# Kernel tuning notes

Hardware: AMD Instinct MI355X
Metric: run time of the kernel (lower is better)

Reference implementation:

```python
import jax, jax.numpy as jnp
import numpy as np

B, NX, NY, H = 4096, 64, 64, 256
ITERS = 20
REG = 0.1          # SinkhornScorer reg (stored as log, used as exp(log reg))
TEMP = 0.1         # SinkhornScorer temperature
ALPHA_BOTH = -100.0
LN_EPS = 1e-5


def setup_inputs() -> dict:
    key = jax.random.key(0)
    k1, k2, k3 = jax.random.split(key, 3)
    return {
        "x": jax.random.normal(k1, (B, NX, H), dtype=jnp.float32),
        "y": jax.random.normal(k2, (B, NY, H), dtype=jnp.float32),
        "ln_gamma": jnp.ones((H,), dtype=jnp.float32),
        "ln_beta": jnp.zeros((H,), dtype=jnp.float32),
        "w_db": jax.random.normal(k3, (H, 1), dtype=jnp.float32) * 0.05,
        "b_db": jnp.zeros((1,), dtype=jnp.float32),
    }


def _layer_norm(t, g, b):
    mu = jnp.mean(t, axis=-1, keepdims=True)
    var = jnp.mean((t - mu) ** 2, axis=-1, keepdims=True)  # biased, like torch LayerNorm
    return (t - mu) / jnp.sqrt(var + LN_EPS) * g + b


def _l2norm(t):
    n = jnp.sqrt(jnp.sum(t * t, axis=-1, keepdims=True))
    return t / jnp.maximum(n, 1e-12)


def reference(x, y, ln_gamma, ln_beta, w_db, b_db):
    b, m, h = x.shape
    n = y.shape[1]
    log_reg = jnp.log(jnp.float32(REG))
    log_temp = jnp.log(jnp.float32(TEMP))

    # CosineScorer(temperature=1), get_diag=False -> (b, n_x, n_y)
    scores = jnp.einsum("bxh,byh->bxy", _l2norm(x), _l2norm(y))

    # dustbin scores: tanh(Linear(LayerNorm(.))) -> (b, n, 1)
    alpha_x = jnp.tanh(_layer_norm(x, ln_gamma, ln_beta) @ w_db + b_db)  # (b, m, 1)
    alpha_y = jnp.tanh(_layer_norm(y, ln_gamma, ln_beta) @ w_db + b_db)  # (b, n, 1)

    # --- log_optimal_transport (SuperGlue-style with per-element dustbins) ---
    top = jnp.concatenate([scores, alpha_x], axis=2)                     # (b, m, n+1)
    bot = jnp.concatenate(
        [jnp.swapaxes(alpha_y, 1, 2), jnp.full((b, 1, 1), ALPHA_BOTH, scores.dtype)],
        axis=2,
    )                                                                    # (b, 1, n+1)
    couplings = jnp.concatenate([top, bot], axis=1) / jnp.exp(log_reg)   # (b, m+1, n+1)

    norm = -jnp.log(jnp.float32(m + n))
    log_mu = jnp.concatenate(
        [jnp.full((m,), norm), jnp.array([jnp.log(jnp.float32(n)) + norm])]
    )
    log_nu = jnp.concatenate(
        [jnp.full((n,), norm), jnp.array([jnp.log(jnp.float32(m)) + norm])]
    )
    log_mu = jnp.broadcast_to(log_mu, (b, m + 1))
    log_nu = jnp.broadcast_to(log_nu, (b, n + 1))

    def step(carry, _):
        u, v = carry
        u = log_mu - jax.nn.logsumexp(couplings + v[:, None, :], axis=2)
        v = log_nu - jax.nn.logsumexp(couplings + u[:, :, None], axis=1)
        return (u, v), None

    (u, v), _ = jax.lax.scan(
        step, (jnp.zeros_like(log_mu), jnp.zeros_like(log_nu)), None, length=ITERS
    )

    matching = couplings + u[:, :, None] + v[:, None, :] - norm  # log matching, (b, m+1, n+1)
    # per-pair alignment score: expected cosine similarity under the plan, / temperature
    score_out = jnp.sum(jnp.exp(matching[:, :-1, :-1]) * scores, axis=(1, 2)) / jnp.exp(log_temp)
    return matching, score_out
```

## Files before the change

kernel.cpp:

```cpp
#include <hip/hip_runtime.h>

#define NR 64
#define NH 256
#define NP1 65
#define TSTRIDE 68
#define NITER 20

__device__ __forceinline__ float dot4(float4 a, float4 b) {
  return a.x * b.x + a.y * b.y + a.z * b.z + a.w * b.w;
}

__global__ __launch_bounds__(256, 4)
void sinkhorn_kernel(const float* __restrict__ x, const float* __restrict__ y,
                     const float* __restrict__ gam, const float* __restrict__ bet,
                     const float* __restrict__ wdb, const float* __restrict__ bdb,
                     float* __restrict__ out_match, float* __restrict__ out_score)
{
  const int b    = blockIdx.x;
  const int t    = threadIdx.x;
  const int lane = t & 63;
  const int wvid = t >> 6;
  const int ti   = t >> 4;
  const int tj   = t & 15;
  const int i0   = ti * 4, j0 = tj * 4;

  __shared__ __align__(16) float s_buf[2 * NR * TSTRIDE];
  __shared__ __align__(16) float s_gw[NH];
  __shared__ __align__(16) float s_sx[NR], s_ax[NR], s_sy[NR], s_ay[NR];
  __shared__ float s_red[8];
  __shared__ float s_S12[2];

  float* xsT  = s_buf;
  float* ysT  = s_buf + NR * TSTRIDE;
  float* vp   = s_buf;
  float* vp64 = s_buf + 512;

  const float norm_c  = -4.852030263919617f;
  const float logmu64 = -0.6931471805599453f;

  {
    float gv = gam[t];
    float wv = wdb[t];
    float p1 = gv * wv;
    float p2 = bet[t] * wv;
    s_gw[t] = p1;
    #pragma unroll
    for (int o = 1; o < 64; o <<= 1) { p1 += __shfl_xor(p1, o); p2 += __shfl_xor(p2, o); }
    if (lane == 0) { s_red[wvid * 2] = p1; s_red[wvid * 2 + 1] = p2; }
  }
  __syncthreads();
  if (t == 0) {
    s_S12[0] = s_red[0] + s_red[2] + s_red[4] + s_red[6];
    s_S12[1] = s_red[1] + s_red[3] + s_red[5] + s_red[7] + bdb[0];
  }

  float acc[4][4] = {};
  float xsum[4] = {}, xsq[4] = {}, xdg[4] = {};
  float ysum[4] = {}, ysq[4] = {}, ydg[4] = {};

  const size_t gbase = (size_t)b * NR * NH;
  const int lh4 = tj * 4;

  for (int ch = 0; ch < 4; ++ch) {
    __syncthreads();
    const float4 gw4 = *(const float4*)(s_gw + ch * 64 + lh4);
    #pragma unroll
    for (int j = 0; j < 4; ++j) {
      const int row = ti + 16 * j;
      const int wcol = ((((row >> 2) ^ tj) & 15) << 2) + (row & 3);
      const float4 xv = *(const float4*)(x + gbase + (size_t)row * NH + ch * 64 + lh4);
      xsum[j] += xv.x + xv.y + xv.z + xv.w;
      xsq[j]  += dot4(xv, xv);
      xdg[j]  += dot4(xv, gw4);
      xsT[(lh4 + 0) * TSTRIDE + wcol] = xv.x;
      xsT[(lh4 + 1) * TSTRIDE + wcol] = xv.y;
      xsT[(lh4 + 2) * TSTRIDE + wcol] = xv.z;
      xsT[(lh4 + 3) * TSTRIDE + wcol] = xv.w;
      const float4 yv = *(const float4*)(y + gbase + (size_t)row * NH + ch * 64 + lh4);
      ysum[j] += yv.x + yv.y + yv.z + yv.w;
      ysq[j]  += dot4(yv, yv);
      ydg[j]  += dot4(yv, gw4);
      ysT[(lh4 + 0) * TSTRIDE + wcol] = yv.x;
      ysT[(lh4 + 1) * TSTRIDE + wcol] = yv.y;
      ysT[(lh4 + 2) * TSTRIDE + wcol] = yv.z;
      ysT[(lh4 + 3) * TSTRIDE + wcol] = yv.w;
    }
    __syncthreads();
    #pragma unroll 4
    for (int k = 0; k < 64; ++k) {
      const int kb = k >> 2;
      const float4 a4 = *(const float4*)(xsT + k * TSTRIDE + (((ti ^ kb) & 15) << 2));
      const float4 b4 = *(const float4*)(ysT + k * TSTRIDE + (((tj ^ kb) & 15) << 2));
      acc[0][0] += a4.x * b4.x; acc[0][1] += a4.x * b4.y; acc[0][2] += a4.x * b4.z; acc[0][3] += a4.x * b4.w;
      acc[1][0] += a4.y * b4.x; acc[1][1] += a4.y * b4.y; acc[1][2] += a4.y * b4.z; acc[1][3] += a4.y * b4.w;
      acc[2][0] += a4.z * b4.x; acc[2][1] += a4.z * b4.y; acc[2][2] += a4.z * b4.z; acc[2][3] += a4.z * b4.w;
      acc[3][0] += a4.w * b4.x; acc[3][1] += a4.w * b4.y; acc[3][2] += a4.w * b4.z; acc[3][3] += a4.w * b4.w;
    }
  }

  #pragma unroll
  for (int o = 1; o < 16; o <<= 1) {
    #pragma unroll
    for (int j = 0; j < 4; ++j) {
      xsum[j] += __shfl_xor(xsum[j], o);
      xsq[j]  += __shfl_xor(xsq[j], o);
      xdg[j]  += __shfl_xor(xdg[j], o);
      ysum[j] += __shfl_xor(ysum[j], o);
      ysq[j]  += __shfl_xor(ysq[j], o);
      ydg[j]  += __shfl_xor(ydg[j], o);
    }
  }
  {
    if (tj == 0) {
      const float S1 = s_S12[0], S2 = s_S12[1];
      #pragma unroll
      for (int j = 0; j < 4; ++j) {
        const int r = ti + 16 * j;
        float mu   = xsum[j] * (1.0f / NH);
        float var  = xsq[j] * (1.0f / NH) - mu * mu;
        float rstd = rsqrtf(var + 1e-5f);
        s_ax[r] = tanhf(rstd * (xdg[j] - mu * S1) + S2);
        s_sx[r] = 1.0f / fmaxf(sqrtf(xsq[j]), 1e-12f);
        mu   = ysum[j] * (1.0f / NH);
        var  = ysq[j] * (1.0f / NH) - mu * mu;
        rstd = rsqrtf(var + 1e-5f);
        s_ay[r] = tanhf(rstd * (ydg[j] - mu * S1) + S2);
        s_sy[r] = 1.0f / fmaxf(sqrtf(ysq[j]), 1e-12f);
      }
    }
  }
  __syncthreads();

  const float4 sx4 = *(const float4*)(s_sx + i0);
  const float4 sy4 = *(const float4*)(s_sy + j0);
  const float4 ax4 = *(const float4*)(s_ax + i0);
  const float4 ay4 = *(const float4*)(s_ay + j0);
  const float sxr[4] = {sx4.x, sx4.y, sx4.z, sx4.w};
  const float syc[4] = {sy4.x, sy4.y, sy4.z, sy4.w};
  float C[4][4], E[4][4];
  #pragma unroll
  for (int r = 0; r < 4; ++r) {
    #pragma unroll
    for (int c = 0; c < 4; ++c) {
      C[r][c] = acc[r][c] * sxr[r] * syc[c] * 10.0f;
      E[r][c] = __expf(C[r][c]);
    }
  }
  const float exi64[4] = {__expf(10.0f * ax4.x), __expf(10.0f * ax4.y),
                          __expf(10.0f * ax4.z), __expf(10.0f * ax4.w)};
  const float ey64[4]  = {__expf(10.0f * ay4.x), __expf(10.0f * ay4.y),
                          __expf(10.0f * ay4.z), __expf(10.0f * ay4.w)};

  float ev_c[4] = {1.0f, 1.0f, 1.0f, 1.0f};
  float ev64 = 1.0f;
  float eu_r[4];
  float eu64 = 1.0f;
  float su_s[4], p64_s, sv_s[4], rs_s;
  int bufo = 0;

  #pragma unroll 2
  for (int it = 0; it < NITER; ++it) {
    float s0 = E[0][0] * ev_c[0] + E[0][1] * ev_c[1] + E[0][2] * ev_c[2] + E[0][3] * ev_c[3];
    float s1 = E[1][0] * ev_c[0] + E[1][1] * ev_c[1] + E[1][2] * ev_c[2] + E[1][3] * ev_c[3];
    float s2 = E[2][0] * ev_c[0] + E[2][1] * ev_c[1] + E[2][2] * ev_c[2] + E[2][3] * ev_c[3];
    float s3 = E[3][0] * ev_c[0] + E[3][1] * ev_c[1] + E[3][2] * ev_c[2] + E[3][3] * ev_c[3];
    float p64 = ey64[0] * ev_c[0] + ey64[1] * ev_c[1] + ey64[2] * ev_c[2] + ey64[3] * ev_c[3];
    #pragma unroll
    for (int o = 1; o < 16; o <<= 1) {
      s0  += __shfl_xor(s0, o);
      s1  += __shfl_xor(s1, o);
      s2  += __shfl_xor(s2, o);
      s3  += __shfl_xor(s3, o);
      p64 += __shfl_xor(p64, o);
    }
    su_s[0] = s0 + exi64[0] * ev64;
    su_s[1] = s1 + exi64[1] * ev64;
    su_s[2] = s2 + exi64[2] * ev64;
    su_s[3] = s3 + exi64[3] * ev64;
    p64_s = p64;
    eu_r[0] = 0.0078125f * __builtin_amdgcn_rcpf(su_s[0]);
    eu_r[1] = 0.0078125f * __builtin_amdgcn_rcpf(su_s[1]);
    eu_r[2] = 0.0078125f * __builtin_amdgcn_rcpf(su_s[2]);
    eu_r[3] = 0.0078125f * __builtin_amdgcn_rcpf(su_s[3]);
    eu64    = 0.5f       * __builtin_amdgcn_rcpf(p64);

    float q0 = E[0][0] * eu_r[0] + E[1][0] * eu_r[1] + E[2][0] * eu_r[2] + E[3][0] * eu_r[3];
    float q1 = E[0][1] * eu_r[0] + E[1][1] * eu_r[1] + E[2][1] * eu_r[2] + E[3][1] * eu_r[3];
    float q2 = E[0][2] * eu_r[0] + E[1][2] * eu_r[1] + E[2][2] * eu_r[2] + E[3][2] * eu_r[3];
    float q3 = E[0][3] * eu_r[0] + E[1][3] * eu_r[1] + E[2][3] * eu_r[2] + E[3][3] * eu_r[3];
    float r64 = exi64[0] * eu_r[0] + exi64[1] * eu_r[1] + exi64[2] * eu_r[2] + exi64[3] * eu_r[3];
    #pragma unroll
    for (int o = 16; o < 64; o <<= 1) {
      q0  += __shfl_xor(q0, o);
      q1  += __shfl_xor(q1, o);
      q2  += __shfl_xor(q2, o);
      q3  += __shfl_xor(q3, o);
      r64 += __shfl_xor(r64, o);
    }
    if ((t & 48) == 0) {
      *(float4*)(vp + (bufo * 4 + wvid) * 64 + j0) = make_float4(q0, q1, q2, q3);
      if (tj == 0) vp64[bufo * 4 + wvid] = r64;
    }
    __syncthreads();
    float sv0 = 0.0f, sv1 = 0.0f, sv2 = 0.0f, sv3 = 0.0f;
    #pragma unroll
    for (int w = 0; w < 4; ++w) {
      const float4 qq = *(const float4*)(vp + (bufo * 4 + w) * 64 + j0);
      sv0 += qq.x; sv1 += qq.y; sv2 += qq.z; sv3 += qq.w;
    }
    const float4 rr4 = *(const float4*)(vp64 + bufo * 4);
    rs_s = rr4.x + rr4.y + rr4.z + rr4.w;
    sv_s[0] = sv0 + ey64[0] * eu64;
    sv_s[1] = sv1 + ey64[1] * eu64;
    sv_s[2] = sv2 + ey64[2] * eu64;
    sv_s[3] = sv3 + ey64[3] * eu64;
    ev_c[0] = 0.0078125f * __builtin_amdgcn_rcpf(sv_s[0]);
    ev_c[1] = 0.0078125f * __builtin_amdgcn_rcpf(sv_s[1]);
    ev_c[2] = 0.0078125f * __builtin_amdgcn_rcpf(sv_s[2]);
    ev_c[3] = 0.0078125f * __builtin_amdgcn_rcpf(sv_s[3]);
    ev64    = 0.5f       * __builtin_amdgcn_rcpf(rs_s);
    bufo ^= 1;
  }

  float u_r[4], v_c[4];
  #pragma unroll
  for (int r = 0; r < 4; ++r) u_r[r] = norm_c - __logf(su_s[r]);
  #pragma unroll
  for (int c = 0; c < 4; ++c) v_c[c] = norm_c - __logf(sv_s[c]);
  const float u64 = logmu64 - __logf(p64_s);
  const float v64 = logmu64 - __logf(rs_s);

  float sacc = 0.0f;
  const size_t mbase = (size_t)b * (size_t)(NP1 * NP1);
  #pragma unroll
  for (int r = 0; r < 4; ++r) {
    const float m0 = C[r][0] + u_r[r] + v_c[0] - norm_c;
    const float m1 = C[r][1] + u_r[r] + v_c[1] - norm_c;
    const float m2 = C[r][2] + u_r[r] + v_c[2] - norm_c;
    const float m3 = C[r][3] + u_r[r] + v_c[3] - norm_c;
    *(float4*)(out_match + mbase + (size_t)(i0 + r) * NP1 + j0) = make_float4(m0, m1, m2, m3);
    sacc += __expf(m0) * C[r][0] + __expf(m1) * C[r][1]
          + __expf(m2) * C[r][2] + __expf(m3) * C[r][3];
  }
  if (t < 16) {
    const float4 ayv = *(const float4*)(s_ay + j0);
    *(float4*)(out_match + mbase + (size_t)64 * NP1 + j0) = make_float4(
        10.0f * ayv.x + u64 + v_c[0] - norm_c,
        10.0f * ayv.y + u64 + v_c[1] - norm_c,
        10.0f * ayv.z + u64 + v_c[2] - norm_c,
        10.0f * ayv.w + u64 + v_c[3] - norm_c);
  }
  if (tj == 0) {
    const float4 axv = *(const float4*)(s_ax + i0);
    out_match[mbase + (size_t)(i0 + 0) * NP1 + 64] = 10.0f * axv.x + u_r[0] + v64 - norm_c;
    out_match[mbase + (size_t)(i0 + 1) * NP1 + 64] = 10.0f * axv.y + u_r[1] + v64 - norm_c;
    out_match[mbase + (size_t)(i0 + 2) * NP1 + 64] = 10.0f * axv.z + u_r[2] + v64 - norm_c;
    out_match[mbase + (size_t)(i0 + 3) * NP1 + 64] = 10.0f * axv.w + u_r[3] + v64 - norm_c;
  }
  if (t == 0) {
    out_match[mbase + (size_t)64 * NP1 + 64] = -1000.0f + u64 + v64 - norm_c;
  }

  #pragma unroll
  for (int o = 1; o < 64; o <<= 1) sacc += __shfl_xor(sacc, o);
  if (lane == 0) s_red[wvid] = sacc;
  __syncthreads();
  if (t == 0) out_score[b] = s_red[0] + s_red[1] + s_red[2] + s_red[3];
}

extern "C" void kernel_launch(void* const* d_in, const int* in_sizes, int n_in,
                              void* d_out, int out_size, void* d_ws, size_t ws_size,
                              hipStream_t stream) {
  const float* x   = (const float*)d_in[0];
  const float* y   = (const float*)d_in[1];
  const float* gam = (const float*)d_in[2];
  const float* bet = (const float*)d_in[3];
  const float* wdb = (const float*)d_in[4];
  const float* bdb = (const float*)d_in[5];
  float* out_match = (float*)d_out;
  float* out_score = (float*)d_out + (size_t)4096 * 4225;
  sinkhorn_kernel<<<4096, 256, 0, stream>>>(x, y, gam, bet, wdb, bdb, out_match, out_score);
}
```

Measured before the change: 720.2 us.

## Use fp16 MFMA for cosine scores and stage match output through LDS

Replaces the scalar fp32 outer-product loop for x·yᵀ with fp16 16x16x32 MFMA instructions. Operands are converted to half precision and stored in a swizzled row-major LDS layout, and the accumulators are scattered back to an LDS tile so each thread can keep its old 4x4 ownership. The full 65x65 log-matching block is then written to LDS first and streamed out with coalesced scalar stores, replacing the unaligned float4 global stores. Launch bounds are raised to 6 blocks per CU. The fp16 inputs add rounding error to scores that are scaled by 10 before exponentiation, which risks exceeding accuracy tolerance.

```diff
diff --git a/kernel.cpp b/kernel.cpp
--- a/kernel.cpp
+++ b/kernel.cpp
@@ -3,14 +3,17 @@
 #define NR 64
 #define NH 256
 #define NP1 65
-#define TSTRIDE 68
 #define NITER 20
+
+typedef _Float16 f16x8 __attribute__((ext_vector_type(8)));
+typedef _Float16 f16x4 __attribute__((ext_vector_type(4)));
+typedef float f32x4t __attribute__((ext_vector_type(4)));
 
 __device__ __forceinline__ float dot4(float4 a, float4 b) {
   return a.x * b.x + a.y * b.y + a.z * b.z + a.w * b.w;
 }
 
-__global__ __launch_bounds__(256, 4)
+__global__ __launch_bounds__(256, 6)
 void sinkhorn_kernel(const float* __restrict__ x, const float* __restrict__ y,
                      const float* __restrict__ gam, const float* __restrict__ bet,
                      const float* __restrict__ wdb, const float* __restrict__ bdb,
@@ -23,17 +26,21 @@
   const int ti   = t >> 4;
   const int tj   = t & 15;
   const int i0   = ti * 4, j0 = tj * 4;
-
-  __shared__ __align__(16) float s_buf[2 * NR * TSTRIDE];
+  const int ql   = lane >> 4;
+  const int pl   = lane & 15;
+
+  __shared__ __align__(16) float s_buf[4872];
   __shared__ __align__(16) float s_gw[NH];
   __shared__ __align__(16) float s_sx[NR], s_ax[NR], s_sy[NR], s_ay[NR];
   __shared__ float s_red[8];
   __shared__ float s_S12[2];
 
-  float* xsT  = s_buf;
-  float* ysT  = s_buf + NR * TSTRIDE;
-  float* vp   = s_buf;
-  float* vp64 = s_buf + 512;
+  _Float16* As = (_Float16*)s_buf;
+  _Float16* Bs = (_Float16*)s_buf + 4096;
+  float* Cf   = s_buf;
+  float* vp   = s_buf + 4352;
+  float* vp64 = s_buf + 4864;
+  float* Om   = s_buf;
 
   const float norm_c  = -4.852030263919617f;
   const float logmu64 = -0.6931471805599453f;
@@ -54,9 +61,14 @@
     s_S12[1] = s_red[1] + s_red[3] + s_red[5] + s_red[7] + bdb[0];
   }
 
-  float acc[4][4] = {};
   float xsum[4] = {}, xsq[4] = {}, xdg[4] = {};
   float ysum[4] = {}, ysq[4] = {}, ydg[4] = {};
+  f32x4t acc4[4];
+  #pragma unroll
+  for (int ct = 0; ct < 4; ++ct) {
+    #pragma unroll
+    for (int r = 0; r < 4; ++r) acc4[ct][r] = 0.0f;
+  }
 
   const size_t gbase = (size_t)b * NR * NH;
   const int lh4 = tj * 4;
@@ -66,35 +78,39 @@
     const float4 gw4 = *(const float4*)(s_gw + ch * 64 + lh4);
     #pragma unroll
     for (int j = 0; j < 4; ++j) {
-      const int row = ti + 16 * j;
-      const int wcol = ((((row >> 2) ^ tj) & 15) << 2) + (row & 3);
+      const int row  = ti + 16 * j;
+      const int blk  = (tj >> 1) ^ (row & 7);
+      const int boff = row * 128 + blk * 16 + (tj & 1) * 8;
       const float4 xv = *(const float4*)(x + gbase + (size_t)row * NH + ch * 64 + lh4);
       xsum[j] += xv.x + xv.y + xv.z + xv.w;
       xsq[j]  += dot4(xv, xv);
       xdg[j]  += dot4(xv, gw4);
-      xsT[(lh4 + 0) * TSTRIDE + wcol] = xv.x;
-      xsT[(lh4 + 1) * TSTRIDE + wcol] = xv.y;
-      xsT[(lh4 + 2) * TSTRIDE + wcol] = xv.z;
-      xsT[(lh4 + 3) * TSTRIDE + wcol] = xv.w;
+      f16x4 xh;
+      xh[0] = (_Float16)xv.x; xh[1] = (_Float16)xv.y;
+      xh[2] = (_Float16)xv.z; xh[3] = (_Float16)xv.w;
+      *(f16x4*)((char*)As + boff) = xh;
       const float4 yv = *(const float4*)(y + gbase + (size_t)row * NH + ch * 64 + lh4);
       ysum[j] += yv.x + yv.y + yv.z + yv.w;
       ysq[j]  += dot4(yv, yv);
       ydg[j]  += dot4(yv, gw4);
-      ysT[(lh4 + 0) * TSTRIDE + wcol] = yv.x;
-      ysT[(lh4 + 1) * TSTRIDE + wcol] = yv.y;
-      ysT[(lh4 + 2) * TSTRIDE + wcol] = yv.z;
-      ysT[(lh4 + 3) * TSTRIDE + wcol] = yv.w;
+      f16x4 yh;
+      yh[0] = (_Float16)yv.x; yh[1] = (_Float16)yv.y;
+      yh[2] = (_Float16)yv.z; yh[3] = (_Float16)yv.w;
+      *(f16x4*)((char*)Bs + boff) = yh;
     }
     __syncthreads();
-    #pragma unroll 4
-    for (int k = 0; k < 64; ++k) {
-      const int kb = k >> 2;
-      const float4 a4 = *(const float4*)(xsT + k * TSTRIDE + (((ti ^ kb) & 15) << 2));
-      const float4 b4 = *(const float4*)(ysT + k * TSTRIDE + (((tj ^ kb) & 15) << 2));
-      acc[0][0] += a4.x * b4.x; acc[0][1] += a4.x * b4.y; acc[0][2] += a4.x * b4.z; acc[0][3] += a4.x * b4.w;
-      acc[1][0] += a4.y * b4.x; acc[1][1] += a4.y * b4.y; acc[1][2] += a4.y * b4.z; acc[1][3] += a4.y * b4.w;
-      acc[2][0] += a4.z * b4.x; acc[2][1] += a4.z * b4.y; acc[2][2] += a4.z * b4.z; acc[2][3] += a4.z * b4.w;
-      acc[3][0] += a4.w * b4.x; acc[3][1] += a4.w * b4.y; acc[3][2] += a4.w * b4.z; acc[3][3] += a4.w * b4.w;
+    #pragma unroll
+    for (int s = 0; s < 2; ++s) {
+      const int arow = 16 * wvid + pl;
+      const int kb   = 4 * s + ql;
+      const int ab   = kb ^ (pl & 7);
+      const f16x8 af = *(const f16x8*)((char*)As + arow * 128 + ab * 16);
+      #pragma unroll
+      for (int ct = 0; ct < 4; ++ct) {
+        const int bcol = 16 * ct + pl;
+        const f16x8 bf = *(const f16x8*)((char*)Bs + bcol * 128 + ab * 16);
+        acc4[ct] = __builtin_amdgcn_mfma_f32_16x16x32_f16(af, bf, acc4[ct], 0, 0, 0);
+      }
     }
   }
 
@@ -110,23 +126,30 @@
       ydg[j]  += __shfl_xor(ydg[j], o);
     }
   }
-  {
-    if (tj == 0) {
-      const float S1 = s_S12[0], S2 = s_S12[1];
-      #pragma unroll
-      for (int j = 0; j < 4; ++j) {
-        const int r = ti + 16 * j;
-        float mu   = xsum[j] * (1.0f / NH);
-        float var  = xsq[j] * (1.0f / NH) - mu * mu;
-        float rstd = rsqrtf(var + 1e-5f);
-        s_ax[r] = tanhf(rstd * (xdg[j] - mu * S1) + S2);
-        s_sx[r] = 1.0f / fmaxf(sqrtf(xsq[j]), 1e-12f);
-        mu   = ysum[j] * (1.0f / NH);
-        var  = ysq[j] * (1.0f / NH) - mu * mu;
-        rstd = rsqrtf(var + 1e-5f);
-        s_ay[r] = tanhf(rstd * (ydg[j] - mu * S1) + S2);
-        s_sy[r] = 1.0f / fmaxf(sqrtf(ysq[j]), 1e-12f);
-      }
+  if (tj == 0) {
+    const float S1 = s_S12[0], S2 = s_S12[1];
+    #pragma unroll
+    for (int j = 0; j < 4; ++j) {
+      const int r = ti + 16 * j;
+      float mu   = xsum[j] * (1.0f / NH);
+      float var  = xsq[j] * (1.0f / NH) - mu * mu;
+      float rstd = rsqrtf(var + 1e-5f);
+      s_ax[r] = tanhf(rstd * (xdg[j] - mu * S1) + S2);
+      s_sx[r] = 1.0f / fmaxf(sqrtf(xsq[j]), 1e-12f);
+      mu   = ysum[j] * (1.0f / NH);
+      var  = ysq[j] * (1.0f / NH) - mu * mu;
+      rstd = rsqrtf(var + 1e-5f);
+      s_ay[r] = tanhf(rstd * (ydg[j] - mu * S1) + S2);
+      s_sy[r] = 1.0f / fmaxf(sqrtf(ysq[j]), 1e-12f);
+    }
+  }
+  __syncthreads();
+
+  #pragma unroll
+  for (int ct = 0; ct < 4; ++ct) {
+    #pragma unroll
+    for (int r = 0; r < 4; ++r) {
+      Cf[(16 * wvid + 4 * ql + r) * 68 + 16 * ct + pl] = acc4[ct][r];
     }
   }
   __syncthreads();
@@ -140,9 +163,11 @@
   float C[4][4], E[4][4];
   #pragma unroll
   for (int r = 0; r < 4; ++r) {
+    const float4 c4 = *(const float4*)(Cf + (i0 + r) * 68 + j0);
+    const float cr[4] = {c4.x, c4.y, c4.z, c4.w};
     #pragma unroll
     for (int c = 0; c < 4; ++c) {
-      C[r][c] = acc[r][c] * sxr[r] * syc[c] * 10.0f;
+      C[r][c] = cr[c] * sxr[r] * syc[c] * 10.0f;
       E[r][c] = __expf(C[r][c]);
     }
   }
@@ -231,40 +256,40 @@
   const float v64 = logmu64 - __logf(rs_s);
 
   float sacc = 0.0f;
-  const size_t mbase = (size_t)b * (size_t)(NP1 * NP1);
   #pragma unroll
   for (int r = 0; r < 4; ++r) {
-    const float m0 = C[r][0] + u_r[r] + v_c[0] - norm_c;
-    const float m1 = C[r][1] + u_r[r] + v_c[1] - norm_c;
-    const float m2 = C[r][2] + u_r[r] + v_c[2] - norm_c;
-    const float m3 = C[r][3] + u_r[r] + v_c[3] - norm_c;
-    *(float4*)(out_match + mbase + (size_t)(i0 + r) * NP1 + j0) = make_float4(m0, m1, m2, m3);
-    sacc += __expf(m0) * C[r][0] + __expf(m1) * C[r][1]
-          + __expf(m2) * C[r][2] + __expf(m3) * C[r][3];
+    #pragma unroll
+    for (int c = 0; c < 4; ++c) {
+      const float m = C[r][c] + u_r[r] + v_c[c] - norm_c;
+      Om[(i0 + r) * NP1 + (j0 + c)] = m;
+      sacc += __expf(m) * C[r][c];
+    }
   }
   if (t < 16) {
-    const float4 ayv = *(const float4*)(s_ay + j0);
-    *(float4*)(out_match + mbase + (size_t)64 * NP1 + j0) = make_float4(
-        10.0f * ayv.x + u64 + v_c[0] - norm_c,
-        10.0f * ayv.y + u64 + v_c[1] - norm_c,
-        10.0f * ayv.z + u64 + v_c[2] - norm_c,
-        10.0f * ayv.w + u64 + v_c[3] - norm_c);
+    Om[64 * NP1 + j0 + 0] = 10.0f * ay4.x + u64 + v_c[0] - norm_c;
+    Om[64 * NP1 + j0 + 1] = 10.0f * ay4.y + u64 + v_c[1] - norm_c;
+    Om[64 * NP1 + j0 + 2] = 10.0f * ay4.z + u64 + v_c[2] - norm_c;
+    Om[64 * NP1 + j0 + 3] = 10.0f * ay4.w + u64 + v_c[3] - norm_c;
   }
   if (tj == 0) {
-    const float4 axv = *(const float4*)(s_ax + i0);
-    out_match[mbase + (size_t)(i0 + 0) * NP1 + 64] = 10.0f * axv.x + u_r[0] + v64 - norm_c;
-    out_match[mbase + (size_t)(i0 + 1) * NP1 + 64] = 10.0f * axv.y + u_r[1] + v64 - norm_c;
-    out_match[mbase + (size_t)(i0 + 2) * NP1 + 64] = 10.0f * axv.z + u_r[2] + v64 - norm_c;
-    out_match[mbase + (size_t)(i0 + 3) * NP1 + 64] = 10.0f * axv.w + u_r[3] + v64 - norm_c;
+    Om[(i0 + 0) * NP1 + 64] = 10.0f * ax4.x + u_r[0] + v64 - norm_c;
+    Om[(i0 + 1) * NP1 + 64] = 10.0f * ax4.y + u_r[1] + v64 - norm_c;
+    Om[(i0 + 2) * NP1 + 64] = 10.0f * ax4.z + u_r[2] + v64 - norm_c;
+    Om[(i0 + 3) * NP1 + 64] = 10.0f * ax4.w + u_r[3] + v64 - norm_c;
   }
   if (t == 0) {
-    out_match[mbase + (size_t)64 * NP1 + 64] = -1000.0f + u64 + v64 - norm_c;
+    Om[64 * NP1 + 64] = -1000.0f + u64 + v64 - norm_c;
   }
 
   #pragma unroll
   for (int o = 1; o < 64; o <<= 1) sacc += __shfl_xor(sacc, o);
   if (lane == 0) s_red[wvid] = sacc;
   __syncthreads();
+
+  const size_t mbase = (size_t)b * (size_t)(NP1 * NP1);
+  for (int idx = t; idx < NP1 * NP1; idx += 256) {
+    out_match[mbase + idx] = Om[idx];
+  }
   if (t == 0) out_score[b] = s_red[0] + s_red[1] + s_red[2] + s_red[3];
 }
 
```

New measurement: 874.6 us. 1.21x slower.
